# Optimization experiments

Hardware: AMD Instinct MI355X
Metric: run time of the kernel (lower is better)

Reference implementation:

```python
import jax, jax.numpy as jnp
import numpy as np

CURVS = (-1.0, 0.0, 1.0, -0.5)
N, E, B = 50000, 800000, 128
IN, HID, OUT, GHID = 128, 128, 128, 32
K = len(CURVS)
TAU_MIN, TAU_MAX = 0.05, 10.0
EPS = 1e-15


def _vnorm(x):
    return jnp.maximum(jnp.linalg.norm(x, axis=-1, keepdims=True), EPS)


def tan_k(x, k):
    if k > 0:
        sk = np.sqrt(k)
        return jnp.tan(x * sk) / sk
    if k < 0:
        sk = np.sqrt(-k)
        return jnp.tanh(x * sk) / sk
    return x


def artan_k(x, k):
    if k > 0:
        sk = np.sqrt(k)
        return jnp.arctan(x * sk) / sk
    if k < 0:
        sk = np.sqrt(-k)
        return jnp.arctanh(jnp.clip(x * sk, -1.0 + 1e-7, 1.0 - 1e-7)) / sk
    return x


def project(x, k):
    # clip inside Poincare ball for k<0; identity otherwise (geoopt Stereographic.projx)
    if k < 0:
        maxn = (1.0 - 1e-5) / np.sqrt(-k)
        n = _vnorm(x)
        return jnp.where(n > maxn, x * (maxn / n), x)
    return x


def expmap0(u, k):
    n = _vnorm(u)
    return project(tan_k(n, k) * u / n, k)


def logmap0(y, k):
    n = _vnorm(y)
    return artan_k(n, k) * y / n


def mobius_add(x, y, k):
    x2 = jnp.sum(x * x, -1, keepdims=True)
    y2 = jnp.sum(y * y, -1, keepdims=True)
    xy = jnp.sum(x * y, -1, keepdims=True)
    num = (1.0 - 2.0 * k * xy - k * y2) * x + (1.0 + k * x2) * y
    den = jnp.maximum(1.0 - 2.0 * k * xy + k * k * x2 * y2, 1e-15)
    return project(num / den, k)


def mobius_matvec(W, x, k):
    mx = x @ W.T
    if k == 0:
        return mx
    xn = _vnorm(x)
    mxn = _vnorm(mx)
    res = tan_k(mxn / xn * artan_k(xn, k), k) * mx / mxn
    res = jnp.where(jnp.sum(jnp.abs(mx), -1, keepdims=True) == 0.0, 0.0, res)
    return project(res, k)


def dist(x, y, k):
    return 2.0 * artan_k(_vnorm(mobius_add(-x, y, k)), k)[..., 0]


def setup_inputs():
    key = jax.random.key(0)
    ks = jax.random.split(key, 12)
    x = jax.random.normal(ks[0], (N, IN), jnp.float32)
    edge_index = jax.random.randint(ks[1], (2, E), 0, N)
    batch = jnp.sort(jax.random.randint(ks[2], (N,), 0, B))
    s1 = float(np.sqrt(2.0 / (IN + HID)))
    s2 = float(np.sqrt(2.0 / (HID + OUT)))
    sg1 = float(np.sqrt(2.0 / (IN + GHID)))
    sg2 = float(np.sqrt(2.0 / (GHID + OUT)))
    raw0 = float(np.log(np.expm1(1.0 - TAU_MIN)))
    return {
        "x": x,
        "edge_index": edge_index,
        "batch": batch,
        "expert_w1": jax.random.normal(ks[3], (K, HID, IN), jnp.float32) * s1,
        "expert_b1": jnp.zeros((K, HID), jnp.float32),
        "expert_w2": jax.random.normal(ks[4], (K, OUT, HID), jnp.float32) * s2,
        "expert_b2": jnp.zeros((K, OUT), jnp.float32),
        "gate_w1": jax.random.normal(ks[5], (GHID, IN), jnp.float32) * sg1,
        "gate_b1": jnp.zeros((GHID,), jnp.float32),
        "gate_w2": jax.random.normal(ks[6], (OUT, GHID), jnp.float32) * sg2,
        "gate_b2": jnp.zeros((OUT,), jnp.float32),
        "gate_u": jax.random.normal(ks[7], (K, OUT), jnp.float32) * 0.02,
        "tau_raw": jnp.full((K,), raw0, jnp.float32),
    }


def _graph_norm(edge_index):
    loops = jnp.arange(N)
    row = jnp.concatenate([edge_index[0], loops])
    col = jnp.concatenate([edge_index[1], loops])
    deg = jax.ops.segment_sum(jnp.ones(E + N, jnp.float32), col, num_segments=N)
    dinv = deg ** -0.5  # deg >= 1 due to self loops
    return row, col, dinv[row] * dinv[col]


def _kappa_conv(xm, W, b, row, col, enorm, k):
    h = mobius_matvec(W, xm, k)
    bias_pt = expmap0(b[None, :], k)  # proju at origin is identity
    h = mobius_add(h, bias_pt, k)
    t = logmap0(h, k)  # [N, out]
    agg = jax.ops.segment_sum(enorm[:, None] * t[row], col, num_segments=N)
    return expmap0(agg, k)


def reference(x, edge_index, batch, expert_w1, expert_b1, expert_w2, expert_b2,
              gate_w1, gate_b1, gate_w2, gate_b2, gate_u, tau_raw):
    x = x.astype(jnp.float32)
    row, col, enorm = _graph_norm(edge_index)
    counts = jnp.maximum(
        jax.ops.segment_sum(jnp.ones(N, jnp.float32), batch, num_segments=B), 1.0)[:, None]

    # --- Riemannian experts ---
    embs = []
    for i, kv in enumerate(CURVS):
        xm = expmap0(x, kv)  # manifold init (proju at origin = identity)
        xm = _kappa_conv(xm, expert_w1[i], expert_b1[i], row, col, enorm, kv)
        xm = _kappa_conv(xm, expert_w2[i], expert_b2[i], row, col, enorm, kv)
        z = logmap0(xm, kv)
        embs.append(jax.ops.segment_sum(z, batch, num_segments=B) / counts)
    features = jnp.concatenate(embs, axis=-1)  # [B, K*OUT]

    # --- Euclidean gating encoder (GCN) ---
    def gcn(h, W, b):
        m = (h @ W.T)
        out = jax.ops.segment_sum(enorm[:, None] * m[row], col, num_segments=N) + b
        return jax.nn.relu(out)

    g = gcn(x, gate_w1, gate_b1)
    g = gcn(g, gate_w2, gate_b2)
    hgate = jax.ops.segment_sum(g, batch, num_segments=B) / counts  # [B, OUT]

    # --- Geometric distance gate ---
    tau = jnp.clip(jax.nn.softplus(tau_raw) + TAU_MIN, TAU_MIN, TAU_MAX)
    dists = []
    for i, kv in enumerate(CURVS):
        zk = expmap0(hgate, kv)
        yk = expmap0(gate_u[i][None, :], kv)
        dists.append(dist(zk, yk, kv))
    dists = jnp.stack(dists, axis=-1)  # [B, K]
    weights = jax.nn.softmax(-dists / tau[None, :], axis=-1)

    scaled = features * jnp.repeat(weights, OUT, axis=1)
    return scaled, weights, dists, tau
```

## Files before the change

kernel.cpp:

```cpp
#include <hip/hip_runtime.h>
#include <math.h>

#define NN 50000
#define EE 800000
#define ETOT (EE + NN)
#define BB 128
#define DIM 128
#define GHID 32
#define CHUNK 128
#define NCHUNK ((ETOT + CHUNK - 1) / CHUNK)
#define SCB 196

typedef _Float16 f16;
typedef _Float16 f16x2 __attribute__((ext_vector_type(2)));
typedef _Float16 f16x8 __attribute__((ext_vector_type(8)));
typedef float f32x4 __attribute__((ext_vector_type(4)));

struct CurvPack {
  float k[4], sk[4], mx[4];
};

__device__ __forceinline__ float wsum64(float v) {
#pragma unroll
  for (int m = 32; m; m >>= 1) v += __shfl_xor(v, m, 64);
  return v;
}

__device__ __forceinline__ float tan_k_d(float x, float kv, float sk) {
  if (kv > 0.f) return tanf(x * sk) / sk;
  if (kv < 0.f) return tanhf(x * sk) / sk;
  return x;
}

__device__ __forceinline__ float artan_k_d(float x, float kv, float sk) {
  if (kv > 0.f) return atanf(x * sk) / sk;
  if (kv < 0.f) {
    float t = x * sk;
    t = fminf(fmaxf(t, -1.f + 1e-7f), 1.f - 1e-7f);
    return atanhf(t) / sk;
  }
  return x;
}
// ... 112 lines not shown
    int mid = (lo + hi) >> 1;
    if (bnode[mid] < v) lo = mid + 1; else hi = mid;
  }
  bslot[g] = lo;
}

__device__ __forceinline__ bool span_head(const int* bnode, const int* bslot, const int* off,
                                          int g, int& nd) {
  if (bslot[g] != g) return false;
  nd = bnode[g];
  int s = off[nd], e = off[nd + 1];
  return (s / CHUNK) != ((e - 1) / CHUNK);
}

__global__ void k_zeroc(const int* __restrict__ bnode, const int* __restrict__ bslot,
                        const int* __restrict__ off, float* __restrict__ aggc, int nchunk) {
  int g = blockIdx.x * 4 + (threadIdx.x >> 6);
  int lane = threadIdx.x & 63;
  if (g >= nchunk) return;
  int nd;
  if (!span_head(bnode, bslot, off, g, nd)) return;
  float2 z = make_float2(0.f, 0.f);
#pragma unroll
  for (int i = 0; i < 4; i++) ((float2*)aggc)[(size_t)g * 256 + i * 64 + lane] = z;
}

__global__ void k_place(const int* __restrict__ ei, const float* __restrict__ dinv,
                        int* __restrict__ cursor, int2* __restrict__ esw, int e, int n) {
  int i = blockIdx.x * 256 + threadIdx.x;
  int et = e + n;
  if (i >= et) return;
  int r_, c_;
  if (i < e) {
    r_ = ei[i];
    c_ = ei[e + i];
  } else {
    r_ = i - e;
    c_ = i - e;
  }
  int p = atomicAdd(&cursor[c_], 1);
  esw[p] = make_int2(r_, __float_as_int(dinv[r_] * dinv[c_]));
}

__global__ void k_nodeprep(const float* __restrict__ x, float* __restrict__ scl,
                           float* __restrict__ xnk, int n, CurvPack cp) {
  int wid = blockIdx.x * 4 + (threadIdx.x >> 6);
  int lane = threadIdx.x & 63;
  if (wid >= n) return;
  float2 v = ((const float2*)x)[(size_t)wid * 64 + lane];
  float n2 = wsum64(v.x * v.x + v.y * v.y);
  float nraw = sqrtf(n2);
  if (lane < 4) {
    float kv = cp.k[lane], sk = cp.sk[lane], maxn = cp.mx[lane];
    float nnv = fmaxf(nraw, 1e-15f);
    float tk = tan_k_d(nnv, kv, sk);
    float s = tk / nnv;
    float pn = fmaxf(fabsf(tk) * (nraw / nnv), 1e-15f);
    float ps = proj_scale_d(pn, kv, maxn);
    scl[(size_t)lane * n + wid] = s * ps;
    xnk[(size_t)lane * n + wid] = pn * ps;
  }
}

__global__ void k_biaspt_all(const float* __restrict__ eb1, const float* __restrict__ eb2,
                             float* __restrict__ biasb, CurvPack cp) {
  __shared__ float l2[2];
  int blk = blockIdx.x;
  int ex = blk >> 1, layer = blk & 1;
  float kv = cp.k[ex], sk = cp.sk[ex], maxn = cp.mx[ex];
  const float* b = (layer ? eb2 : eb1) + ex * 128;
  float* outb = biasb + blk * 132;
  int j = threadIdx.x;
  float v = b[j];
  float n2 = wsum64(v * v);
  if ((j & 63) == 0) l2[j >> 6] = n2;
  __syncthreads();
  n2 = l2[0] + l2[1];
  float nraw = sqrtf(n2);
  float nnv = fmaxf(nraw, 1e-15f);
  float tk = tan_k_d(nnv, kv, sk);
  float s = tk / nnv;
  float pn = fmaxf(fabsf(tk) * (nraw / nnv), 1e-15f);
  float ps = proj_scale_d(pn, kv, maxn);
  float bp = ps * s * v;
  outb[j] = bp;
  float y2v = wsum64(bp * bp);
  __syncthreads();
  if ((j & 63) == 0) l2[j >> 6] = y2v;
  __syncthreads();
  if (j == 0) outb[128] = l2[0] + l2[1];
}

__global__ void k_w2h(const float* __restrict__ ew1, const float* __restrict__ ew2,
                      f16* __restrict__ whi, f16* __restrict__ wlo) {
  int i = blockIdx.x * 256 + threadIdx.x;
  if (i >= 8 * 16384) return;
  int slot = i >> 14;
  int r = i & 16383;
  int ex = slot >> 1, layer = slot & 1;
  float w = (layer ? ew2 : ew1)[ex * 16384 + r];
  f16 h = (f16)w;
  whi[i] = h;
  wlo[i] = (f16)(w - (float)h);
}

__global__ __launch_bounds__(256) void k_matmfma(
    const float* __restrict__ A, int astr, int aoffPerEx, const float* __restrict__ sclB,
    const float* __restrict__ xnkB, const f16* __restrict__ whiB,
    const f16* __restrict__ wloB, const float* __restrict__ biasB, int layer,
    f16* __restrict__ tout, int n, CurvPack cp) {
  __shared__ float red[3][16][4];
  __shared__ float redT[16][4];
  __shared__ float nAs[16], nCs[16], nL[16];
  int ex = blockIdx.y;
  float kv = cp.k[ex], sk = cp.sk[ex], maxn = cp.mx[ex];
  const f16* whi = whiB + (size_t)(ex * 2 + layer) * 16384;
  const f16* wlo = wloB + (size_t)(ex * 2 + layer) * 16384;
  const float* biasb = biasB + (ex * 2 + layer) * 132;
  const float* scale = sclB + (size_t)ex * n;
  const float* xnorm = xnkB + (size_t)ex * n;

  int tid = threadIdx.x;
  int w = tid >> 6;
  int lane = tid & 63;
  int col = lane & 15;
  int quad = lane >> 4;
  int n0w = blockIdx.x * 16;
  if (n0w >= n) return;

  int anodec = min(n0w + col, n - 1);
  const float* arow = A + (size_t)anodec * astr + ex * aoffPerEx;
  int jt0 = w * 2;

  f32x4 acc[2];
  acc[0] = (f32x4){0.f, 0.f, 0.f, 0.f};
  acc[1] = (f32x4){0.f, 0.f, 0.f, 0.f};

#pragma unroll
  for (int kc = 0; kc < 4; kc++) {
    int kb = kc * 32 + quad * 8;
    float4 a0 = *(const float4*)(arow + kb);
    float4 a1 = *(const float4*)(arow + kb + 4);
    float av[8] = {a0.x, a0.y, a0.z, a0.w, a1.x, a1.y, a1.z, a1.w};
    f16x8 Ah, Al;
#pragma unroll
    for (int i = 0; i < 8; i++) {
      f16 h = (f16)av[i];
      Ah[i] = h;
      Al[i] = (f16)(av[i] - (float)h);
    }
#pragma unroll
    for (int j2 = 0; j2 < 2; j2++) {
      const f16* bh = whi + (size_t)((jt0 + j2) * 16 + col) * 128 + kb;
      const f16* bl = wlo + (size_t)((jt0 + j2) * 16 + col) * 128 + kb;
      f16x8 Bh = *(const f16x8*)bh;
      f16x8 Bl = *(const f16x8*)bl;
      acc[j2] = __builtin_amdgcn_mfma_f32_16x16x32_f16(Ah, Bh, acc[j2], 0, 0, 0);
      acc[j2] = __builtin_amdgcn_mfma_f32_16x16x32_f16(Ah, Bl, acc[j2], 0, 0, 0);
      acc[j2] = __builtin_amdgcn_mfma_f32_16x16x32_f16(Al, Bh, acc[j2], 0, 0, 0);
    }
  }

  float bpj[2];
  bpj[0] = biasb[jt0 * 16 + col];
  bpj[1] = biasb[(jt0 + 1) * 16 + col];
  float y2 = biasb[128];

#pragma unroll
  for (int r = 0; r < 4; r++) {
    float s0 = 0.f, s1 = 0.f, s2 = 0.f;
#pragma unroll
    for (int j2 = 0; j2 < 2; j2++) {
      float v = acc[j2][r];
      s0 = fmaf(v, v, s0);
      s1 += fabsf(v);
      s2 = fmaf(v, bpj[j2], s2);
    }
#pragma unroll
    for (int m = 1; m < 16; m <<= 1) {
      s0 += __shfl_xor(s0, m, 64);
      s1 += __shfl_xor(s1, m, 64);
      s2 += __shfl_xor(s2, m, 64);
    }
    if (col == 0) {
      red[0][quad * 4 + r][w] = s0;
      red[1][quad * 4 + r][w] = s1;
      red[2][quad * 4 + r][w] = s2;
    }
  }
  __syncthreads();

  if (tid < 16) {
    int gnode = min(n0w + tid, n - 1);
    float sc = scale[gnode];
    float s0f = (red[0][tid][0] + red[0][tid][1] + red[0][tid][2] + red[0][tid][3]) * sc * sc;
    float s1f = (red[1][tid][0] + red[1][tid][1] + red[1][tid][2] + red[1][tid][3]) * fabsf(sc);
    float s2f = (red[2][tid][0] + red[2][tid][1] + red[2][tid][2] + red[2][tid][3]) * sc;
    float xnr = xnorm[gnode];
    float xn = fmaxf(xnr, 1e-15f);
    float mxraw = sqrtf(s0f);
    float mxv = fmaxf(mxraw, 1e-15f);
    float ar = artan_k_d(xn, kv, sk);
    float c1 = tan_k_d(mxv / xn * ar, kv, sk);
    float s = (s1f == 0.f) ? 0.f : c1 / mxv;
    float pn = fmaxf(fabsf(c1) * (mxraw / mxv), 1e-15f);
    float ps = (s1f == 0.f) ? 1.f : proj_scale_d(pn, kv, maxn);
    s *= ps;
    float x2 = (s * s) * s0f;
    float xy = s * s2f;
    float Aa = 1.f - 2.f * kv * xy - kv * y2;
    float Cc = 1.f + kv * x2;
    float den = fmaxf(1.f - 2.f * kv * xy + (kv * kv) * x2 * y2, 1e-15f);
    nAs[tid] = Aa * s / den * sc;
    nCs[tid] = Cc / den;
  }
  __syncthreads();

#pragma unroll
  for (int r = 0; r < 4; r++) {
    int idx = quad * 4 + r;
    float Asc = nAs[idx], Cs = nCs[idx];
// ... 4 lines not shown
      t0 = fmaf(v, v, t0);
    }
#pragma unroll
    for (int m = 1; m < 16; m <<= 1) t0 += __shfl_xor(t0, m, 64);
    if (col == 0) redT[idx][w] = t0;
  }
  __syncthreads();

  if (tid < 16) {
    float t0f = redT[tid][0] + redT[tid][1] + redT[tid][2] + redT[tid][3];
    float nraw = sqrtf(t0f);
    float ps2 = proj_scale_d(fmaxf(nraw, 1e-15f), kv, maxn);
    float nh = fmaxf(ps2 * nraw, 1e-15f);
    nL[tid] = artan_k_d(nh, kv, sk) / nh * ps2;
  }
  __syncthreads();

#pragma unroll
  for (int r = 0; r < 4; r++) {
    int idx = quad * 4 + r;
    int gnode = n0w + idx;
    if (gnode >= n) continue;
    float Asc = nAs[idx], Cs = nCs[idx], L = nL[idx];
    f16* trow = tout + (size_t)gnode * 512 + ex * 128;
#pragma unroll
    for (int j2 = 0; j2 < 2; j2++) {
      float v = fmaf(Asc, acc[j2][r], Cs * bpj[j2]);
      trow[(jt0 + j2) * 16 + col] = (f16)(L * v);
    }
  }
}

template <int MODE, int NE>
__global__ __launch_bounds__(256) void k_aggF(
    const int2* __restrict__ esw, const int* __restrict__ off,
    const int* __restrict__ bnode, const int* __restrict__ bslot,
    const int* __restrict__ batch, const f16x2* __restrict__ t, float* __restrict__ agg1,
    float* __restrict__ aggc, float* __restrict__ scl2, float* __restrict__ xnk2,
    float* __restrict__ feats, const float* __restrict__ bias, float* __restrict__ hgate,
    int etot, int n, CurvPack cp) {
  int gw = blockIdx.x * 4 + (threadIdx.x >> 6);
  int lane = threadIdx.x & 63;
  int e0 = gw * CHUNK;
  if (e0 >= etot) return;
  int e1 = min(e0 + CHUNK, etot);
  int bnHead = bnode[gw];
  int slotA = bslot[gw];
  int slotB = ((gw + 1) * CHUNK < etot) ? bslot[gw + 1] : slotA;
  int cur = bnHead;
  int runStart = off[cur];
  int eend = off[cur + 1];
  float ax[NE], ay[NE], pax[NE], pay[NE];
#pragma unroll
  for (int e = 0; e < NE; e++) {
    ax[e] = ay[e] = pax[e] = pay[e] = 0.f;
  }
  int bcur = (MODE >= 1) ? batch[cur] : 0;
  float bbx = 0.f, bby = 0.f;
  if (MODE == 2) {
    float2 bb = ((const float2*)bias)[lane];
    bbx = bb.x;
    bby = bb.y;
  }

  auto flushInterior = [&]() {
#pragma unroll
    for (int e = 0; e < NE; e++) {
      if (MODE == 0) {
        ((float2*)agg1)[(size_t)cur * 256 + e * 64 + lane] = make_float2(ax[e], ay[e]);
        float n2 = wsum64(fmaf(ax[e], ax[e], ay[e] * ay[e]));
        float nraw = sqrtf(n2);
        float nnv = fmaxf(nraw, 1e-15f);
        float tk = tan_k_d(nnv, cp.k[e], cp.sk[e]);
        float s = tk / nnv;
        float pn = fmaxf(fabsf(tk) * (nraw / nnv), 1e-15f);
        float ps = proj_scale_d(pn, cp.k[e], cp.mx[e]);
        if (lane == 0) {
          scl2[(size_t)e * n + cur] = s * ps;
          xnk2[(size_t)e * n + cur] = pn * ps;
        }
      } else if (MODE == 1) {
        float n2 = wsum64(fmaf(ax[e], ax[e], ay[e] * ay[e]));
        float nraw = sqrtf(n2);
        float nnv = fmaxf(nraw, 1e-15f);
        float tk = tan_k_d(nnv, cp.k[e], cp.sk[e]);
        float s = tk / nnv;
        float pn = fmaxf(fabsf(tk) * (nraw / nnv), 1e-15f);
        float ps = proj_scale_d(pn, cp.k[e], cp.mx[e]);
        s *= ps;
        float nh = fmaxf(pn * ps, 1e-15f);
        float sc = artan_k_d(nh, cp.k[e], cp.sk[e]) / nh * s;
        pax[e] = fmaf(sc, ax[e], pax[e]);
        pay[e] = fmaf(sc, ay[e], pay[e]);
      } else {
        pax[e] += fmaxf(ax[e] + bbx, 0.f);
        pay[e] += fmaxf(ay[e] + bby, 0.f);
      }
    }
  };
  auto flushBoundary = [&]() {
    int slot = (cur == bnHead) ? slotA : slotB;
#pragma unroll
    for (int e = 0; e < NE; e++) {
      float* dp = aggc + (size_t)slot * 512 + e * 128 + lane * 2;
      atomicAdd(dp, ax[e]);
      atomicAdd(dp + 1, ay[e]);
    }
  };
  auto flushPool = [&]() {
#pragma unroll
    for (int e = 0; e < NE; e++) {
      if (MODE == 1) {
        float* fp = &feats[(size_t)bcur * 512 + e * 128 + lane * 2];
        atomicAdd(fp, pax[e]);
        atomicAdd(fp + 1, pay[e]);
      } else if (MODE == 2) {
        float* hp = &hgate[(size_t)bcur * 128 + lane * 2];
        atomicAdd(hp, pax[e]);
        atomicAdd(hp + 1, pay[e]);
      }
    }
  };

  int j = e0;
  while (j < e1) {
    if (j + 8 <= e1 && eend >= j + 8) {
      int2 m[8];
#pragma unroll
      for (int q = 0; q < 8; q++) m[q] = esw[j + q];
      f16x2 r[8][NE];
#pragma unroll
      for (int q = 0; q < 8; q++) {
        int s = __builtin_amdgcn_readfirstlane(m[q].x);
        const f16x2* base = t + (size_t)s * 256;
#pragma unroll
        for (int e = 0; e < NE; e++) r[q][e] = base[e * 64 + lane];
      }
#pragma unroll
      for (int q = 0; q < 8; q++) {
        float w = __int_as_float(m[q].y);
#pragma unroll
        for (int e = 0; e < NE; e++) {
          ax[e] = fmaf(w, (float)r[q][e][0], ax[e]);
          ay[e] = fmaf(w, (float)r[q][e][1], ay[e]);
        }
      }
      j += 8;
    } else if (j + 4 <= e1 && eend >= j + 4) {
      int2 m[4];
#pragma unroll
      for (int q = 0; q < 4; q++) m[q] = esw[j + q];
      f16x2 r[4][NE];
#pragma unroll
      for (int q = 0; q < 4; q++) {
        int s = __builtin_amdgcn_readfirstlane(m[q].x);
        const f16x2* base = t + (size_t)s * 256;
#pragma unroll
        for (int e = 0; e < NE; e++) r[q][e] = base[e * 64 + lane];
      }
#pragma unroll
      for (int q = 0; q < 4; q++) {
        float w = __int_as_float(m[q].y);
#pragma unroll
        for (int e = 0; e < NE; e++) {
          ax[e] = fmaf(w, (float)r[q][e][0], ax[e]);
          ay[e] = fmaf(w, (float)r[q][e][1], ay[e]);
        }
      }
      j += 4;
    } else {
      if (j == eend) {
        if (runStart >= e0) flushInterior(); else flushBoundary();
#pragma unroll
        for (int e = 0; e < NE; e++) ax[e] = ay[e] = 0.f;
        runStart = j;
        cur++;
        eend = off[cur + 1];
        if (MODE >= 1) {
          int nb = batch[cur];
          if (nb != bcur) {
            flushPool();
#pragma unroll
            for (int e = 0; e < NE; e++) pax[e] = pay[e] = 0.f;
            bcur = nb;
          }
        }
      }
      int2 m = esw[j];
      int s = __builtin_amdgcn_readfirstlane(m.x);
      const f16x2* base = t + (size_t)s * 256;
      float w = __int_as_float(m.y);
#pragma unroll
      for (int e = 0; e < NE; e++) {
        f16x2 rv = base[e * 64 + lane];
        ax[e] = fmaf(w, (float)rv[0], ax[e]);
        ay[e] = fmaf(w, (float)rv[1], ay[e]);
      }
      j++;
    }
  }
  if (runStart >= e0 && eend <= e1) flushInterior(); else flushBoundary();
  if (MODE >= 1) flushPool();
}

__global__ void k_fix1(const int* __restrict__ bnode, const int* __restrict__ bslot,
                       const int* __restrict__ off, const float* __restrict__ aggc,
                       float* __restrict__ agg1, float* __restrict__ scl2,
                       float* __restrict__ xnk2, int nchunk, int n, CurvPack cp) {
  int g = blockIdx.x * 4 + (threadIdx.x >> 6);
  int lane = threadIdx.x & 63;
  if (g >= nchunk) return;
  int nd;
  if (!span_head(bnode, bslot, off, g, nd)) return;
#pragma unroll
  for (int e = 0; e < 4; e++) {
    float2 v = ((const float2*)aggc)[(size_t)g * 256 + e * 64 + lane];
    ((float2*)agg1)[(size_t)nd * 256 + e * 64 + lane] = v;
    float n2 = wsum64(fmaf(v.x, v.x, v.y * v.y));
    float nraw = sqrtf(n2);
    float nnv = fmaxf(nraw, 1e-15f);
    float tk = tan_k_d(nnv, cp.k[e], cp.sk[e]);
    float s = tk / nnv;
    float pn = fmaxf(fabsf(tk) * (nraw / nnv), 1e-15f);
    float ps = proj_scale_d(pn, cp.k[e], cp.mx[e]);
    if (lane == 0) {
      scl2[(size_t)e * n + nd] = s * ps;
      xnk2[(size_t)e * n + nd] = pn * ps;
    }
  }
}

__global__ void k_fix2(const int* __restrict__ bnode, const int* __restrict__ bslot,
                       const int* __restrict__ off, const float* __restrict__ aggc,
                       const int* __restrict__ batch, float* __restrict__ feats, int nchunk,
                       CurvPack cp) {
  int g = blockIdx.x * 4 + (threadIdx.x >> 6);
  int lane = threadIdx.x & 63;
  if (g >= nchunk) return;
  int nd;
  if (!span_head(bnode, bslot, off, g, nd)) return;
  int b = batch[nd];
#pragma unroll
  for (int e = 0; e < 4; e++) {
    float2 v = ((const float2*)aggc)[(size_t)g * 256 + e * 64 + lane];
    float n2 = wsum64(fmaf(v.x, v.x, v.y * v.y));
    float nraw = sqrtf(n2);
    float nnv = fmaxf(nraw, 1e-15f);
    float tk = tan_k_d(nnv, cp.k[e], cp.sk[e]);
    float s = tk / nnv;
    float pn = fmaxf(fabsf(tk) * (nraw / nnv), 1e-15f);
    float ps = proj_scale_d(pn, cp.k[e], cp.mx[e]);
    s *= ps;
    float nh = fmaxf(pn * ps, 1e-15f);
    float sc = artan_k_d(nh, cp.k[e], cp.sk[e]) / nh * s;
    float* fp = &feats[(size_t)b * 512 + e * 128 + lane * 2];
    atomicAdd(fp, sc * v.x);
    atomicAdd(fp + 1, sc * v.y);
  }
}

__global__ void k_fixG(const int* __restrict__ bnode, const int* __restrict__ bslot,
                       const int* __restrict__ off, const float* __restrict__ aggc,
                       const int* __restrict__ batch, const float* __restrict__ bias,
                       float* __restrict__ hgate, int nchunk) {
  int g = blockIdx.x * 4 + (threadIdx.x >> 6);
  int lane = threadIdx.x & 63;
  if (g >= nchunk) return;
  int nd;
  if (!span_head(bnode, bslot, off, g, nd)) return;
  float2 v = ((const float2*)aggc)[(size_t)g * 256 + lane];
  float2 bb = ((const float2*)bias)[lane];
  int b = batch[nd];
  float* hp = &hgate[(size_t)b * 128 + lane * 2];
  atomicAdd(hp, fmaxf(v.x + bb.x, 0.f));
  atomicAdd(hp + 1, fmaxf(v.y + bb.y, 0.f));
}

__global__ __launch_bounds__(256) void k_gate1(const float* __restrict__ x,
                                               const float* __restrict__ gw1,
                                               float* __restrict__ m1, int n) {
  __shared__ float xT[64][68];
  __shared__ float Wt[64][36];
  int tid = threadIdx.x;
  int n0 = blockIdx.x * 64;
  int c = tid & 7, r = tid >> 3;
  float acc[2][4];
#pragma unroll
  for (int i = 0; i < 2; i++)
#pragma unroll
    for (int jj = 0; jj < 4; jj++) acc[i][jj] = 0.f;

  for (int kc = 0; kc < 2; kc++) {
    if (kc) __syncthreads();
#pragma unroll
    for (int it = 0; it < 8; it++) {
      int u = tid + it * 256;
      int j = u >> 6, kd = u & 63;
      Wt[kd][j] = gw1[j * 128 + kc * 64 + kd];
// ... 61 lines not shown
    xT[4 * c4 + 2][node] = v.z;
    xT[4 * c4 + 3][node] = v.w;
  }
  __syncthreads();
#pragma unroll 8
  for (int kd = 0; kd < 32; kd++) {
    float4 av = *(const float4*)&xT[kd][r * 4];
    float4 b0 = *(const float4*)&Wt[kd][c * 8];
    float4 b1 = *(const float4*)&Wt[kd][c * 8 + 4];
    float a[4] = {av.x, av.y, av.z, av.w};
    float bbv[8] = {b0.x, b0.y, b0.z, b0.w, b1.x, b1.y, b1.z, b1.w};
#pragma unroll
    for (int i = 0; i < 4; i++)
#pragma unroll
      for (int jj = 0; jj < 8; jj++) acc[i][jj] = fmaf(a[i], bbv[jj], acc[i][jj]);
  }
#pragma unroll
  for (int i = 0; i < 4; i++) {
    int node = n0 + r * 4 + i;
    if (node >= n) continue;
    f16x8 hv;
#pragma unroll
    for (int jj = 0; jj < 8; jj++) hv[jj] = (f16)acc[i][jj];
    *((f16x8*)(m2 + (size_t)node * 512) + c) = hv;
  }
}

__global__ void k_agg_relu32(const float* __restrict__ m1, const int* __restrict__ off,
                             const int2* __restrict__ esw, const float* __restrict__ bias,
                             float* __restrict__ g1, int n) {
  int node = blockIdx.x * 4 + (threadIdx.x >> 6);
  int lane = threadIdx.x & 63;
  if (node >= n) return;
  int grp = lane >> 3, l8 = lane & 7;
  int e0 = off[node], e1 = off[node + 1];
  float4 acc = make_float4(0.f, 0.f, 0.f, 0.f);
  for (int base = e0 + grp; base < e1; base += 8) {
    int2 me = esw[base];
    int ss = me.x;
    float ww = __int_as_float(me.y);
    float4 tv = ((const float4*)m1)[(size_t)ss * 8 + l8];
    acc.x = fmaf(ww, tv.x, acc.x);
    acc.y = fmaf(ww, tv.y, acc.y);
    acc.z = fmaf(ww, tv.z, acc.z);
    acc.w = fmaf(ww, tv.w, acc.w);
  }
#pragma unroll
  for (int m = 8; m <= 32; m <<= 1) {
    acc.x += __shfl_xor(acc.x, m, 64);
    acc.y += __shfl_xor(acc.y, m, 64);
    acc.z += __shfl_xor(acc.z, m, 64);
    acc.w += __shfl_xor(acc.w, m, 64);
  }
  if (grp == 0) {
    float4 bb = ((const float4*)bias)[l8];
    float4 o = make_float4(fmaxf(acc.x + bb.x, 0.f), fmaxf(acc.y + bb.y, 0.f),
                           fmaxf(acc.z + bb.z, 0.f), fmaxf(acc.w + bb.w, 0.f));
    ((float4*)g1)[(size_t)node * 8 + l8] = o;
  }
}

__global__ __launch_bounds__(128) void k_final(const float* __restrict__ feats,
                                               const float* __restrict__ hgate,
                                               const float* __restrict__ counts,
                                               const float* __restrict__ gate_u,
                                               const float* __restrict__ tau_raw,
                                               float* __restrict__ out, CurvPack cp) {
  __shared__ float l2[2];
  int b = blockIdx.x;
  int j = threadIdx.x;
  float cnt = fmaxf(counts[b], 1.f);
  float hg = hgate[(size_t)b * 128 + j] / cnt;

  auto bsum = [&](float v) -> float {
    v = wsum64(v);
    __syncthreads();
    if ((j & 63) == 0) l2[j >> 6] = v;
    __syncthreads();
    return l2[0] + l2[1];
  };

// ... 71 lines not shown
                              void* d_out, int out_size, void* d_ws, size_t ws_size,
                              hipStream_t stream) {
  const float* x = (const float*)d_in[0];
  const int* ei = (const int*)d_in[1];
  const int* batch = (const int*)d_in[2];
  const float* ew1 = (const float*)d_in[3];
  const float* eb1 = (const float*)d_in[4];
  const float* ew2 = (const float*)d_in[5];
  const float* eb2 = (const float*)d_in[6];
  const float* gw1 = (const float*)d_in[7];
  const float* gb1 = (const float*)d_in[8];
  const float* gw2 = (const float*)d_in[9];
  const float* gb2 = (const float*)d_in[10];
  const float* gu = (const float*)d_in[11];
  const float* traw = (const float*)d_in[12];
  float* out = (float*)d_out;

  const int N = NN, E = EE, ET = ETOT, B = BB;

  float* ws = (float*)d_ws;
  size_t o = 0;
  f16* t4 = (f16*)ws;       o += (size_t)N * 256;
  float* agg1 = ws + o;     o += (size_t)N * 512;
  float* aggc = ws + o;     o += (size_t)NCHUNK * 512;
  float* deg = ws + o;      o += N;
  float* scl1 = ws + o;     o += (size_t)4 * N;
  float* xnk1 = ws + o;     o += (size_t)4 * N;
  float* scl2 = ws + o;     o += (size_t)4 * N;
  float* xnk2 = ws + o;     o += (size_t)4 * N;
  float* counts = ws + o;   o += 256;
  float* feats = ws + o;    o += (size_t)B * 512;
  float* hg = ws + o;       o += (size_t)B * 128;
  float* biasb = ws + o;    o += 8 * 132;
  f16* whi = (f16*)(ws + o);    o += 8 * 16384 / 2;
  f16* wlo = (f16*)(ws + o);    o += 8 * 16384 / 2;
  int* ideg = (int*)(ws + o);   o += N;
  int* csroff = (int*)(ws + o); o += N + 8;
  int* cursor = (int*)(ws + o); o += N;
  int* boff = (int*)(ws + o);   o += 136;
  int* bsum = (int*)(ws + o);   o += 256;
  int* bnode = (int*)(ws + o);  o += NCHUNK + 8;
  int* bslot = (int*)(ws + o);  o += NCHUNK + 8;
  int2* esw = (int2*)(ws + o);  o += (size_t)2 * ET;

  float* m1 = agg1;
  float* g1 = agg1 + (size_t)N * 32;

  hipMemsetAsync(counts, 0, (256 + (size_t)B * 512 + (size_t)B * 128) * sizeof(float), stream);

  const double curvs[4] = {-1.0, 0.0, 1.0, -0.5};
  CurvPack cp;
  for (int i = 0; i < 4; i++) {
    double kd = curvs[i];
    double skd = sqrt(fabs(kd));
    cp.k[i] = (float)kd;
    cp.sk[i] = (float)skd;
    cp.mx[i] = (kd < 0) ? (float)((1.0 - 1e-5) / skd) : 3.0e38f;
  }

  k_init<<<(N + 255) / 256, 256, 0, stream>>>(deg, N);
  k_counts<<<1, 256, 0, stream>>>(batch, boff, counts, N);
  k_deg<<<(E + 255) / 256, 256, 0, stream>>>(ei, deg, E);
  k_dinv<<<(N + 255) / 256, 256, 0, stream>>>(deg, ideg, N);
  k_scanA<<<SCB, 256, 0, stream>>>(ideg, bsum, N);
  k_scanB<<<1, 256, 0, stream>>>(bsum, SCB);
  k_scanC<<<SCB, 256, 0, stream>>>(ideg, bsum, csroff, cursor, N);
  k_bnodes<<<(NCHUNK + 255) / 256, 256, 0, stream>>>(csroff, bnode, NCHUNK, N);
  k_bslot<<<(NCHUNK + 255) / 256, 256, 0, stream>>>(bnode, bslot, NCHUNK);
  k_place<<<(ET + 255) / 256, 256, 0, stream>>>(ei, deg, cursor, esw, E, N);
  k_nodeprep<<<(N + 3) / 4, 256, 0, stream>>>(x, scl1, xnk1, N, cp);
  k_biaspt_all<<<8, 128, 0, stream>>>(eb1, eb2, biasb, cp);
  k_w2h<<<512, 256, 0, stream>>>(ew1, ew2, whi, wlo);

  const int aggBlocks = (NCHUNK + 3) / 4;
  dim3 mfmaGrid((N + 15) / 16, 4);

  k_matmfma<<<mfmaGrid, 256, 0, stream>>>(x, 128, 0, scl1, xnk1, whi, wlo, biasb, 0, t4, N, cp);
  k_zeroc<<<aggBlocks, 256, 0, stream>>>(bnode, bslot, csroff, aggc, NCHUNK);
  k_aggF<0, 4><<<aggBlocks, 256, 0, stream>>>(esw, csroff, bnode, bslot, batch,
                                              (const f16x2*)t4, agg1, aggc, scl2, xnk2, nullptr,
                                              nullptr, nullptr, ET, N, cp);
  k_fix1<<<aggBlocks, 256, 0, stream>>>(bnode, bslot, csroff, aggc, agg1, scl2, xnk2, NCHUNK, N,
                                        cp);
  k_matmfma<<<mfmaGrid, 256, 0, stream>>>(agg1, 512, 128, scl2, xnk2, whi, wlo, biasb, 1, t4, N,
                                          cp);
  k_zeroc<<<aggBlocks, 256, 0, stream>>>(bnode, bslot, csroff, aggc, NCHUNK);
  k_aggF<1, 4><<<aggBlocks, 256, 0, stream>>>(esw, csroff, bnode, bslot, batch,
                                              (const f16x2*)t4, nullptr, aggc, nullptr, nullptr,
                                              feats, nullptr, nullptr, ET, N, cp);
  k_fix2<<<aggBlocks, 256, 0, stream>>>(bnode, bslot, csroff, aggc, batch, feats, NCHUNK, cp);

  k_gate1<<<(N + 63) / 64, 256, 0, stream>>>(x, gw1, m1, N);
  k_agg_relu32<<<(N + 3) / 4, 256, 0, stream>>>(m1, csroff, esw, gb1, g1, N);
  k_gate2<<<(N + 63) / 64, 256, 0, stream>>>(g1, gw2, t4, N);
  k_zeroc<<<aggBlocks, 256, 0, stream>>>(bnode, bslot, csroff, aggc, NCHUNK);
  k_aggF<2, 1><<<aggBlocks, 256, 0, stream>>>(esw, csroff, bnode, bslot, batch,
                                              (const f16x2*)t4, nullptr, aggc, nullptr, nullptr,
                                              nullptr, gb2, hg, ET, N, cp);
  k_fixG<<<aggBlocks, 256, 0, stream>>>(bnode, bslot, csroff, aggc, batch, gb2, hg, NCHUNK);

  k_final<<<B, 128, 0, stream>>>(feats, hg, counts, gu, traw, out, cp);

  (void)in_sizes; (void)n_in; (void)out_size; (void)ws_size;
}
```

Before: 1.016 ms.

## Fuse gate GCN aggregation into expert aggregation passes with interleaved feature layout

The Euclidean gate GCN's neighbour aggregations now run inside the two expert aggregation kernels, sharing the same edge walk. This removes the separate k_agg_relu32, gate-mode k_aggF and k_fixG launches and one full pass over the edge list. Per-node norms for the expmap scale are now computed inside the MFMA matmul instead of a separate prep kernel, which drops the scl/xnk buffers. The t4 output is interleaved so each lane fetches one 16-byte vector holding all four experts per neighbour. Edge metadata is loaded once per 8 edges and broadcast with readlane. When a node's norm is below a threshold where logmap(expmap(v)) is the identity, the transcendental round trip is skipped. This adds register pressure and more atomics in the boundary path.

```diff
diff --git a/kernel.cpp b/kernel.cpp
--- a/kernel.cpp
+++ b/kernel.cpp
@@ -17,7 +17,7 @@
 typedef float f32x4 __attribute__((ext_vector_type(4)));
 
 struct CurvPack {
-  float k[4], sk[4], mx[4];
+  float k[4], sk[4], mx[4], thr2[4];
 };
 
 __device__ __forceinline__ float wsum64(float v) {
@@ -176,7 +176,7 @@
   if (!span_head(bnode, bslot, off, g, nd)) return;
   float2 z = make_float2(0.f, 0.f);
 #pragma unroll
-  for (int i = 0; i < 4; i++) ((float2*)aggc)[(size_t)g * 256 + i * 64 + lane] = z;
+  for (int i = 0; i < 5; i++) ((float2*)aggc)[(size_t)g * 320 + i * 64 + lane] = z;
 }
 
 __global__ void k_place(const int* __restrict__ ei, const float* __restrict__ dinv,
@@ -196,26 +196,6 @@
   esw[p] = make_int2(r_, __float_as_int(dinv[r_] * dinv[c_]));
 }
 
-__global__ void k_nodeprep(const float* __restrict__ x, float* __restrict__ scl,
-                           float* __restrict__ xnk, int n, CurvPack cp) {
-  int wid = blockIdx.x * 4 + (threadIdx.x >> 6);
-  int lane = threadIdx.x & 63;
-  if (wid >= n) return;
-  float2 v = ((const float2*)x)[(size_t)wid * 64 + lane];
-  float n2 = wsum64(v.x * v.x + v.y * v.y);
-  float nraw = sqrtf(n2);
-  if (lane < 4) {
-    float kv = cp.k[lane], sk = cp.sk[lane], maxn = cp.mx[lane];
-    float nnv = fmaxf(nraw, 1e-15f);
-    float tk = tan_k_d(nnv, kv, sk);
-    float s = tk / nnv;
-    float pn = fmaxf(fabsf(tk) * (nraw / nnv), 1e-15f);
-    float ps = proj_scale_d(pn, kv, maxn);
-    scl[(size_t)lane * n + wid] = s * ps;
-    xnk[(size_t)lane * n + wid] = pn * ps;
-  }
-}
-
 __global__ void k_biaspt_all(const float* __restrict__ eb1, const float* __restrict__ eb2,
                              float* __restrict__ biasb, CurvPack cp) {
   __shared__ float l2[2];
@@ -259,10 +239,10 @@
 }
 
 __global__ __launch_bounds__(256) void k_matmfma(
-    const float* __restrict__ A, int astr, int aoffPerEx, const float* __restrict__ sclB,
-    const float* __restrict__ xnkB, const f16* __restrict__ whiB,
-    const f16* __restrict__ wloB, const float* __restrict__ biasB, int layer,
-    f16* __restrict__ tout, int n, CurvPack cp) {
+    const float* __restrict__ A, int astr, int aoffPerEx,
+    const f16* __restrict__ whiB, const f16* __restrict__ wloB,
+    const float* __restrict__ biasB, int layer, f16* __restrict__ tout, int n,
+    CurvPack cp) {
   __shared__ float red[3][16][4];
   __shared__ float redT[16][4];
   __shared__ float nAs[16], nCs[16], nL[16];
@@ -271,8 +251,6 @@
   const f16* whi = whiB + (size_t)(ex * 2 + layer) * 16384;
   const f16* wlo = wloB + (size_t)(ex * 2 + layer) * 16384;
   const float* biasb = biasB + (ex * 2 + layer) * 132;
-  const float* scale = sclB + (size_t)ex * n;
-  const float* xnorm = xnkB + (size_t)ex * n;
 
   int tid = threadIdx.x;
   int w = tid >> 6;
@@ -289,6 +267,7 @@
   f32x4 acc[2];
   acc[0] = (f32x4){0.f, 0.f, 0.f, 0.f};
   acc[1] = (f32x4){0.f, 0.f, 0.f, 0.f};
+  float a_n2 = 0.f;
 
 #pragma unroll
   for (int kc = 0; kc < 4; kc++) {
@@ -299,6 +278,7 @@
     f16x8 Ah, Al;
 #pragma unroll
     for (int i = 0; i < 8; i++) {
+      a_n2 = fmaf(av[i], av[i], a_n2);
       f16 h = (f16)av[i];
       Ah[i] = h;
       Al[i] = (f16)(av[i] - (float)h);
@@ -314,6 +294,8 @@
       acc[j2] = __builtin_amdgcn_mfma_f32_16x16x32_f16(Al, Bh, acc[j2], 0, 0, 0);
     }
   }
+  a_n2 += __shfl_xor(a_n2, 16, 64);
+  a_n2 += __shfl_xor(a_n2, 32, 64);
 
   float bpj[2];
   bpj[0] = biasb[jt0 * 16 + col];
@@ -345,12 +327,17 @@
   __syncthreads();
 
   if (tid < 16) {
-    int gnode = min(n0w + tid, n - 1);
-    float sc = scale[gnode];
+    float nraw0 = sqrtf(a_n2);
+    float nnv0 = fmaxf(nraw0, 1e-15f);
+    float tk0 = tan_k_d(nnv0, kv, sk);
+    float pn0 = fmaxf(fabsf(tk0) * (nraw0 / nnv0), 1e-15f);
+    float ps0 = proj_scale_d(pn0, kv, maxn);
+    float sc = (tk0 / nnv0) * ps0;
+    float xnr = pn0 * ps0;
+
     float s0f = (red[0][tid][0] + red[0][tid][1] + red[0][tid][2] + red[0][tid][3]) * sc * sc;
     float s1f = (red[1][tid][0] + red[1][tid][1] + red[1][tid][2] + red[1][tid][3]) * fabsf(sc);
     float s2f = (red[2][tid][0] + red[2][tid][1] + red[2][tid][2] + red[2][tid][3]) * sc;
-    float xnr = xnorm[gnode];
     float xn = fmaxf(xnr, 1e-15f);
     float mxraw = sqrtf(s0f);
     float mxv = fmaxf(mxraw, 1e-15f);
@@ -401,23 +388,26 @@
     int gnode = n0w + idx;
     if (gnode >= n) continue;
     float Asc = nAs[idx], Cs = nCs[idx], L = nL[idx];
-    f16* trow = tout + (size_t)gnode * 512 + ex * 128;
+    f16* trow = tout + (size_t)gnode * 512;
 #pragma unroll
     for (int j2 = 0; j2 < 2; j2++) {
       float v = fmaf(Asc, acc[j2][r], Cs * bpj[j2]);
-      trow[(jt0 + j2) * 16 + col] = (f16)(L * v);
-    }
-  }
-}
-
-template <int MODE, int NE>
+      int d = (jt0 + j2) * 16 + col;
+      trow[(d >> 1) * 8 + ex * 2 + (d & 1)] = (f16)(L * v);
+    }
+  }
+}
+
+template <int MODE>
 __global__ __launch_bounds__(256) void k_aggF(
     const int2* __restrict__ esw, const int* __restrict__ off,
     const int* __restrict__ bnode, const int* __restrict__ bslot,
-    const int* __restrict__ batch, const f16x2* __restrict__ t, float* __restrict__ agg1,
-    float* __restrict__ aggc, float* __restrict__ scl2, float* __restrict__ xnk2,
-    float* __restrict__ feats, const float* __restrict__ bias, float* __restrict__ hgate,
-    int etot, int n, CurvPack cp) {
+    const int* __restrict__ batch, const f16x8* __restrict__ t,
+    const float* __restrict__ gm1, const f16x2* __restrict__ tg,
+    float* __restrict__ agg1, float* __restrict__ aggc,
+    float* __restrict__ g1, float* __restrict__ feats,
+    const float* __restrict__ gbias, float* __restrict__ hgate,
+    int etot, CurvPack cp) {
   int gw = blockIdx.x * 4 + (threadIdx.x >> 6);
   int lane = threadIdx.x & 63;
   int e0 = gw * CHUNK;
@@ -429,199 +419,163 @@
   int cur = bnHead;
   int runStart = off[cur];
   int eend = off[cur + 1];
-  float ax[NE], ay[NE], pax[NE], pay[NE];
-#pragma unroll
-  for (int e = 0; e < NE; e++) {
-    ax[e] = ay[e] = pax[e] = pay[e] = 0.f;
-  }
-  int bcur = (MODE >= 1) ? batch[cur] : 0;
-  float bbx = 0.f, bby = 0.f;
-  if (MODE == 2) {
-    float2 bb = ((const float2*)bias)[lane];
+  float ax[4], ay[4], pax[4], pay[4];
+#pragma unroll
+  for (int e = 0; e < 4; e++) ax[e] = ay[e] = pax[e] = pay[e] = 0.f;
+  float gx = 0.f, gy = 0.f, pgx = 0.f, pgy = 0.f;
+  int bcur = (MODE == 1) ? batch[cur] : 0;
+  float bbx, bby = 0.f;
+  if (MODE == 0) {
+    bbx = gbias[lane & 31];
+  } else {
+    float2 bb = ((const float2*)gbias)[lane];
     bbx = bb.x;
     bby = bb.y;
   }
 
   auto flushInterior = [&]() {
 #pragma unroll
-    for (int e = 0; e < NE; e++) {
+    for (int e = 0; e < 4; e++) {
       if (MODE == 0) {
         ((float2*)agg1)[(size_t)cur * 256 + e * 64 + lane] = make_float2(ax[e], ay[e]);
+      } else {
         float n2 = wsum64(fmaf(ax[e], ax[e], ay[e] * ay[e]));
-        float nraw = sqrtf(n2);
-        float nnv = fmaxf(nraw, 1e-15f);
-        float tk = tan_k_d(nnv, cp.k[e], cp.sk[e]);
-        float s = tk / nnv;
-        float pn = fmaxf(fabsf(tk) * (nraw / nnv), 1e-15f);
-        float ps = proj_scale_d(pn, cp.k[e], cp.mx[e]);
-        if (lane == 0) {
-          scl2[(size_t)e * n + cur] = s * ps;
-          xnk2[(size_t)e * n + cur] = pn * ps;
+        if (n2 <= cp.thr2[e]) {
+          pax[e] += ax[e];
+          pay[e] += ay[e];
+        } else {
+          float nraw = sqrtf(n2);
+          float nnv = fmaxf(nraw, 1e-15f);
+          float tk = tan_k_d(nnv, cp.k[e], cp.sk[e]);
+          float s = tk / nnv;
+          float pn = fmaxf(fabsf(tk) * (nraw / nnv), 1e-15f);
+          float ps = proj_scale_d(pn, cp.k[e], cp.mx[e]);
+          s *= ps;
+          float nh = fmaxf(pn * ps, 1e-15f);
+          float sc = artan_k_d(nh, cp.k[e], cp.sk[e]) / nh * s;
+          pax[e] = fmaf(sc, ax[e], pax[e]);
+          pay[e] = fmaf(sc, ay[e], pay[e]);
         }
-      } else if (MODE == 1) {
-        float n2 = wsum64(fmaf(ax[e], ax[e], ay[e] * ay[e]));
-        float nraw = sqrtf(n2);
-        float nnv = fmaxf(nraw, 1e-15f);
-        float tk = tan_k_d(nnv, cp.k[e], cp.sk[e]);
-        float s = tk / nnv;
-        float pn = fmaxf(fabsf(tk) * (nraw / nnv), 1e-15f);
-        float ps = proj_scale_d(pn, cp.k[e], cp.mx[e]);
-        s *= ps;
-        float nh = fmaxf(pn * ps, 1e-15f);
-        float sc = artan_k_d(nh, cp.k[e], cp.sk[e]) / nh * s;
-        pax[e] = fmaf(sc, ax[e], pax[e]);
-        pay[e] = fmaf(sc, ay[e], pay[e]);
-      } else {
-        pax[e] += fmaxf(ax[e] + bbx, 0.f);
-        pay[e] += fmaxf(ay[e] + bby, 0.f);
       }
+    }
+    if (MODE == 0) {
+      if (lane < 32) g1[(size_t)cur * 32 + lane] = fmaxf(gx + bbx, 0.f);
+    } else {
+      pgx += fmaxf(gx + bbx, 0.f);
+      pgy += fmaxf(gy + bby, 0.f);
     }
   };
   auto flushBoundary = [&]() {
     int slot = (cur == bnHead) ? slotA : slotB;
-#pragma unroll
-    for (int e = 0; e < NE; e++) {
-      float* dp = aggc + (size_t)slot * 512 + e * 128 + lane * 2;
-      atomicAdd(dp, ax[e]);
-      atomicAdd(dp + 1, ay[e]);
+    float* dp = aggc + (size_t)slot * 640;
+#pragma unroll
+    for (int e = 0; e < 4; e++) {
+      atomicAdd(dp + e * 128 + lane * 2, ax[e]);
+      atomicAdd(dp + e * 128 + lane * 2 + 1, ay[e]);
+    }
+    if (MODE == 0) {
+      if (lane < 32) atomicAdd(dp + 512 + lane, gx);
+    } else {
+      atomicAdd(dp + 512 + lane * 2, gx);
+      atomicAdd(dp + 512 + lane * 2 + 1, gy);
     }
   };
   auto flushPool = [&]() {
 #pragma unroll
-    for (int e = 0; e < NE; e++) {
-      if (MODE == 1) {
-        float* fp = &feats[(size_t)bcur * 512 + e * 128 + lane * 2];
-        atomicAdd(fp, pax[e]);
-        atomicAdd(fp + 1, pay[e]);
-      } else if (MODE == 2) {
-        float* hp = &hgate[(size_t)bcur * 128 + lane * 2];
-        atomicAdd(hp, pax[e]);
-        atomicAdd(hp + 1, pay[e]);
-      }
-    }
+    for (int e = 0; e < 4; e++) {
+      float* fp = &feats[(size_t)bcur * 512 + e * 128 + lane * 2];
+      atomicAdd(fp, pax[e]);
+      atomicAdd(fp + 1, pay[e]);
+    }
+    float* hp = &hgate[(size_t)bcur * 128 + lane * 2];
+    atomicAdd(hp, pgx);
+    atomicAdd(hp + 1, pgy);
   };
 
-  int j = e0;
-  while (j < e1) {
-    if (j + 8 <= e1 && eend >= j + 8) {
-      int2 m[8];
-#pragma unroll
-      for (int q = 0; q < 8; q++) m[q] = esw[j + q];
-      f16x2 r[8][NE];
-#pragma unroll
-      for (int q = 0; q < 8; q++) {
-        int s = __builtin_amdgcn_readfirstlane(m[q].x);
-        const f16x2* base = t + (size_t)s * 256;
-#pragma unroll
-        for (int e = 0; e < NE; e++) r[q][e] = base[e * 64 + lane];
-      }
-#pragma unroll
-      for (int q = 0; q < 8; q++) {
-        float w = __int_as_float(m[q].y);
-#pragma unroll
-        for (int e = 0; e < NE; e++) {
-          ax[e] = fmaf(w, (float)r[q][e][0], ax[e]);
-          ay[e] = fmaf(w, (float)r[q][e][1], ay[e]);
-        }
-      }
-      j += 8;
-    } else if (j + 4 <= e1 && eend >= j + 4) {
-      int2 m[4];
-#pragma unroll
-      for (int q = 0; q < 4; q++) m[q] = esw[j + q];
-      f16x2 r[4][NE];
-#pragma unroll
-      for (int q = 0; q < 4; q++) {
-        int s = __builtin_amdgcn_readfirstlane(m[q].x);
-        const f16x2* base = t + (size_t)s * 256;
-#pragma unroll
-        for (int e = 0; e < NE; e++) r[q][e] = base[e * 64 + lane];
-      }
-#pragma unroll
-      for (int q = 0; q < 4; q++) {
-        float w = __int_as_float(m[q].y);
-#pragma unroll
-        for (int e = 0; e < NE; e++) {
-          ax[e] = fmaf(w, (float)r[q][e][0], ax[e]);
-          ay[e] = fmaf(w, (float)r[q][e][1], ay[e]);
-        }
-      }
-      j += 4;
-    } else {
-      if (j == eend) {
+  for (int j = e0; j < e1; j += 8) {
+    int2 mv = esw[j + (lane & 7)];
+    f16x8 rv[8];
+    float gvf[8];
+    f16x2 gvh[8];
+#pragma unroll
+    for (int q = 0; q < 8; q++) {
+      int s = __builtin_amdgcn_readlane(mv.x, q);
+      rv[q] = t[(size_t)s * 64 + lane];
+      if (MODE == 0) gvf[q] = gm1[(size_t)s * 32 + (lane & 31)];
+      else gvh[q] = tg[(size_t)s * 64 + lane];
+    }
+#pragma unroll
+    for (int q = 0; q < 8; q++) {
+      if (j + q == eend) {
         if (runStart >= e0) flushInterior(); else flushBoundary();
 #pragma unroll
-        for (int e = 0; e < NE; e++) ax[e] = ay[e] = 0.f;
-        runStart = j;
+        for (int e = 0; e < 4; e++) ax[e] = ay[e] = 0.f;
+        gx = gy = 0.f;
+        runStart = j + q;
         cur++;
         eend = off[cur + 1];
-        if (MODE >= 1) {
-          int nb = batch[cur];
-          if (nb != bcur) {
+        if (MODE == 1) {
+          int nbt = batch[cur];
+          if (nbt != bcur) {
             flushPool();
 #pragma unroll
-            for (int e = 0; e < NE; e++) pax[e] = pay[e] = 0.f;
-            bcur = nb;
+            for (int e = 0; e < 4; e++) pax[e] = pay[e] = 0.f;
+            pgx = pgy = 0.f;
+            bcur = nbt;
           }
         }
       }
-      int2 m = esw[j];
-      int s = __builtin_amdgcn_readfirstlane(m.x);
-      const f16x2* base = t + (size_t)s * 256;
-      float w = __int_as_float(m.y);
-#pragma unroll
-      for (int e = 0; e < NE; e++) {
-        f16x2 rv = base[e * 64 + lane];
-        ax[e] = fmaf(w, (float)rv[0], ax[e]);
-        ay[e] = fmaf(w, (float)rv[1], ay[e]);
+      float w = __int_as_float(__builtin_amdgcn_readlane(mv.y, q));
+#pragma unroll
+      for (int e = 0; e < 4; e++) {
+        ax[e] = fmaf(w, (float)rv[q][2 * e], ax[e]);
+        ay[e] = fmaf(w, (float)rv[q][2 * e + 1], ay[e]);
       }
-      j++;
+      if (MODE == 0) {
+        gx = fmaf(w, gvf[q], gx);
+      } else {
+        gx = fmaf(w, (float)gvh[q][0], gx);
+        gy = fmaf(w, (float)gvh[q][1], gy);
+      }
     }
   }
   if (runStart >= e0 && eend <= e1) flushInterior(); else flushBoundary();
-  if (MODE >= 1) flushPool();
+  if (MODE == 1) flushPool();
 }
 
 __global__ void k_fix1(const int* __restrict__ bnode, const int* __restrict__ bslot,
                        const int* __restrict__ off, const float* __restrict__ aggc,
-                       float* __restrict__ agg1, float* __restrict__ scl2,
-                       float* __restrict__ xnk2, int nchunk, int n, CurvPack cp) {
+                       float* __restrict__ agg1, float* __restrict__ g1,
+                       const float* __restrict__ gb1, int nchunk) {
   int g = blockIdx.x * 4 + (threadIdx.x >> 6);
   int lane = threadIdx.x & 63;
   if (g >= nchunk) return;
   int nd;
   if (!span_head(bnode, bslot, off, g, nd)) return;
+  const float* sp = aggc + (size_t)g * 640;
 #pragma unroll
   for (int e = 0; e < 4; e++) {
-    float2 v = ((const float2*)aggc)[(size_t)g * 256 + e * 64 + lane];
+    float2 v = ((const float2*)sp)[e * 64 + lane];
     ((float2*)agg1)[(size_t)nd * 256 + e * 64 + lane] = v;
-    float n2 = wsum64(fmaf(v.x, v.x, v.y * v.y));
-    float nraw = sqrtf(n2);
-    float nnv = fmaxf(nraw, 1e-15f);
-    float tk = tan_k_d(nnv, cp.k[e], cp.sk[e]);
-    float s = tk / nnv;
-    float pn = fmaxf(fabsf(tk) * (nraw / nnv), 1e-15f);
-    float ps = proj_scale_d(pn, cp.k[e], cp.mx[e]);
-    if (lane == 0) {
-      scl2[(size_t)e * n + nd] = s * ps;
-      xnk2[(size_t)e * n + nd] = pn * ps;
-    }
-  }
+  }
+  if (lane < 32) g1[(size_t)nd * 32 + lane] = fmaxf(sp[512 + lane] + gb1[lane], 0.f);
 }
 
 __global__ void k_fix2(const int* __restrict__ bnode, const int* __restrict__ bslot,
                        const int* __restrict__ off, const float* __restrict__ aggc,
-                       const int* __restrict__ batch, float* __restrict__ feats, int nchunk,
-                       CurvPack cp) {
+                       const int* __restrict__ batch, float* __restrict__ feats,
+                       const float* __restrict__ gb2, float* __restrict__ hgate,
+                       int nchunk, CurvPack cp) {
   int g = blockIdx.x * 4 + (threadIdx.x >> 6);
   int lane = threadIdx.x & 63;
   if (g >= nchunk) return;
   int nd;
   if (!span_head(bnode, bslot, off, g, nd)) return;
   int b = batch[nd];
+  const float* sp = aggc + (size_t)g * 640;
 #pragma unroll
   for (int e = 0; e < 4; e++) {
-    float2 v = ((const float2*)aggc)[(size_t)g * 256 + e * 64 + lane];
+    float2 v = ((const float2*)sp)[e * 64 + lane];
     float n2 = wsum64(fmaf(v.x, v.x, v.y * v.y));
     float nraw = sqrtf(n2);
     float nnv = fmaxf(nraw, 1e-15f);
@@ -636,23 +590,11 @@
     atomicAdd(fp, sc * v.x);
     atomicAdd(fp + 1, sc * v.y);
   }
-}
-
-__global__ void k_fixG(const int* __restrict__ bnode, const int* __restrict__ bslot,
-                       const int* __restrict__ off, const float* __restrict__ aggc,
-                       const int* __restrict__ batch, const float* __restrict__ bias,
-                       float* __restrict__ hgate, int nchunk) {
-  int g = blockIdx.x * 4 + (threadIdx.x >> 6);
-  int lane = threadIdx.x & 63;
-  if (g >= nchunk) return;
-  int nd;
-  if (!span_head(bnode, bslot, off, g, nd)) return;
-  float2 v = ((const float2*)aggc)[(size_t)g * 256 + lane];
-  float2 bb = ((const float2*)bias)[lane];
-  int b = batch[nd];
+  float2 gv = ((const float2*)(sp + 512))[lane];
+  float2 bb = ((const float2*)gb2)[lane];
   float* hp = &hgate[(size_t)b * 128 + lane * 2];
-  atomicAdd(hp, fmaxf(v.x + bb.x, 0.f));
-  atomicAdd(hp + 1, fmaxf(v.y + bb.y, 0.f));
+  atomicAdd(hp, fmaxf(gv.x + bb.x, 0.f));
+  atomicAdd(hp + 1, fmaxf(gv.y + bb.y, 0.f));
 }
 
 __global__ __launch_bounds__(256) void k_gate1(const float* __restrict__ x,
@@ -760,41 +702,7 @@
     f16x8 hv;
 #pragma unroll
     for (int jj = 0; jj < 8; jj++) hv[jj] = (f16)acc[i][jj];
-    *((f16x8*)(m2 + (size_t)node * 512) + c) = hv;
-  }
-}
-
-__global__ void k_agg_relu32(const float* __restrict__ m1, const int* __restrict__ off,
-                             const int2* __restrict__ esw, const float* __restrict__ bias,
-                             float* __restrict__ g1, int n) {
-  int node = blockIdx.x * 4 + (threadIdx.x >> 6);
-  int lane = threadIdx.x & 63;
-  if (node >= n) return;
-  int grp = lane >> 3, l8 = lane & 7;
-  int e0 = off[node], e1 = off[node + 1];
-  float4 acc = make_float4(0.f, 0.f, 0.f, 0.f);
-  for (int base = e0 + grp; base < e1; base += 8) {
-    int2 me = esw[base];
-    int ss = me.x;
-    float ww = __int_as_float(me.y);
-    float4 tv = ((const float4*)m1)[(size_t)ss * 8 + l8];
-    acc.x = fmaf(ww, tv.x, acc.x);
-    acc.y = fmaf(ww, tv.y, acc.y);
-    acc.z = fmaf(ww, tv.z, acc.z);
-    acc.w = fmaf(ww, tv.w, acc.w);
-  }
-#pragma unroll
-  for (int m = 8; m <= 32; m <<= 1) {
-    acc.x += __shfl_xor(acc.x, m, 64);
-    acc.y += __shfl_xor(acc.y, m, 64);
-    acc.z += __shfl_xor(acc.z, m, 64);
-    acc.w += __shfl_xor(acc.w, m, 64);
-  }
-  if (grp == 0) {
-    float4 bb = ((const float4*)bias)[l8];
-    float4 o = make_float4(fmaxf(acc.x + bb.x, 0.f), fmaxf(acc.y + bb.y, 0.f),
-                           fmaxf(acc.z + bb.z, 0.f), fmaxf(acc.w + bb.w, 0.f));
-    ((float4*)g1)[(size_t)node * 8 + l8] = o;
+    *((f16x8*)(m2 + (size_t)node * 128) + c) = hv;
   }
 }
 
@@ -912,18 +820,17 @@
   size_t o = 0;
   f16* t4 = (f16*)ws;       o += (size_t)N * 256;
   float* agg1 = ws + o;     o += (size_t)N * 512;
-  float* aggc = ws + o;     o += (size_t)NCHUNK * 512;
+  float* aggc = ws + o;     o += (size_t)NCHUNK * 640;
   float* deg = ws + o;      o += N;
-  float* scl1 = ws + o;     o += (size_t)4 * N;
-  float* xnk1 = ws + o;     o += (size_t)4 * N;
-  float* scl2 = ws + o;     o += (size_t)4 * N;
-  float* xnk2 = ws + o;     o += (size_t)4 * N;
   float* counts = ws + o;   o += 256;
   float* feats = ws + o;    o += (size_t)B * 512;
   float* hg = ws + o;       o += (size_t)B * 128;
   float* biasb = ws + o;    o += 8 * 132;
   f16* whi = (f16*)(ws + o);    o += 8 * 16384 / 2;
   f16* wlo = (f16*)(ws + o);    o += 8 * 16384 / 2;
+  float* m1 = ws + o;       o += (size_t)N * 32;
+  float* g1 = ws + o;       o += (size_t)N * 32;
+  f16* tg = (f16*)(ws + o); o += (size_t)N * 64;
   int* ideg = (int*)(ws + o);   o += N;
   int* csroff = (int*)(ws + o); o += N + 8;
   int* cursor = (int*)(ws + o); o += N;
@@ -933,9 +840,6 @@
   int* bslot = (int*)(ws + o);  o += NCHUNK + 8;
   int2* esw = (int2*)(ws + o);  o += (size_t)2 * ET;
 
-  float* m1 = agg1;
-  float* g1 = agg1 + (size_t)N * 32;
-
   hipMemsetAsync(counts, 0, (256 + (size_t)B * 512 + (size_t)B * 128) * sizeof(float), stream);
 
   const double curvs[4] = {-1.0, 0.0, 1.0, -0.5};
@@ -946,6 +850,15 @@
     cp.k[i] = (float)kd;
     cp.sk[i] = (float)skd;
     cp.mx[i] = (kd < 0) ? (float)((1.0 - 1e-5) / skd) : 3.0e38f;
+    if (kd < 0) {
+      double thr = 6.0 / skd;
+      cp.thr2[i] = (float)(thr * thr);
+    } else if (kd > 0) {
+      double thr = 1.5 / skd;
+      cp.thr2[i] = (float)(thr * thr);
+    } else {
+      cp.thr2[i] = 3.0e38f;
+    }
   }
 
   k_init<<<(N + 255) / 256, 256, 0, stream>>>(deg, N);
@@ -958,36 +871,28 @@
   k_bnodes<<<(NCHUNK + 255) / 256, 256, 0, stream>>>(csroff, bnode, NCHUNK, N);
   k_bslot<<<(NCHUNK + 255) / 256, 256, 0, stream>>>(bnode, bslot, NCHUNK);
   k_place<<<(ET + 255) / 256, 256, 0, stream>>>(ei, deg, cursor, esw, E, N);
-  k_nodeprep<<<(N + 3) / 4, 256, 0, stream>>>(x, scl1, xnk1, N, cp);
   k_biaspt_all<<<8, 128, 0, stream>>>(eb1, eb2, biasb, cp);
   k_w2h<<<512, 256, 0, stream>>>(ew1, ew2, whi, wlo);
+  k_gate1<<<(N + 63) / 64, 256, 0, stream>>>(x, gw1, m1, N);
 
   const int aggBlocks = (NCHUNK + 3) / 4;
   dim3 mfmaGrid((N + 15) / 16, 4);
 
-  k_matmfma<<<mfmaGrid, 256, 0, stream>>>(x, 128, 0, scl1, xnk1, whi, wlo, biasb, 0, t4, N, cp);
+  k_matmfma<<<mfmaGrid, 256, 0, stream>>>(x, 128, 0, whi, wlo, biasb, 0, t4, N, cp);
   k_zeroc<<<aggBlocks, 256, 0, stream>>>(bnode, bslot, csroff, aggc, NCHUNK);
-  k_aggF<0, 4><<<aggBlocks, 256, 0, stream>>>(esw, csroff, bnode, bslot, batch,
-                                              (const f16x2*)t4, agg1, aggc, scl2, xnk2, nullptr,
-                                              nullptr, nullptr, ET, N, cp);
-  k_fix1<<<aggBlocks, 256, 0, stream>>>(bnode, bslot, csroff, aggc, agg1, scl2, xnk2, NCHUNK, N,
-                                        cp);
-  k_matmfma<<<mfmaGrid, 256, 0, stream>>>(agg1, 512, 128, scl2, xnk2, whi, wlo, biasb, 1, t4, N,
-                                          cp);
+  k_aggF<0><<<aggBlocks, 256, 0, stream>>>(esw, csroff, bnode, bslot, batch,
+                                           (const f16x8*)t4, m1, nullptr, agg1, aggc, g1,
+                                           nullptr, gb1, nullptr, ET, cp);
+  k_fix1<<<aggBlocks, 256, 0, stream>>>(bnode, bslot, csroff, aggc, agg1, g1, gb1, NCHUNK);
+  k_gate2<<<(N + 63) / 64, 256, 0, stream>>>(g1, gw2, tg, N);
+
+  k_matmfma<<<mfmaGrid, 256, 0, stream>>>(agg1, 512, 128, whi, wlo, biasb, 1, t4, N, cp);
   k_zeroc<<<aggBlocks, 256, 0, stream>>>(bnode, bslot, csroff, aggc, NCHUNK);
-  k_aggF<1, 4><<<aggBlocks, 256, 0, stream>>>(esw, csroff, bnode, bslot, batch,
-                                              (const f16x2*)t4, nullptr, aggc, nullptr, nullptr,
-                                              feats, nullptr, nullptr, ET, N, cp);
-  k_fix2<<<aggBlocks, 256, 0, stream>>>(bnode, bslot, csroff, aggc, batch, feats, NCHUNK, cp);
-
-  k_gate1<<<(N + 63) / 64, 256, 0, stream>>>(x, gw1, m1, N);
-  k_agg_relu32<<<(N + 3) / 4, 256, 0, stream>>>(m1, csroff, esw, gb1, g1, N);
-  k_gate2<<<(N + 63) / 64, 256, 0, stream>>>(g1, gw2, t4, N);
-  k_zeroc<<<aggBlocks, 256, 0, stream>>>(bnode, bslot, csroff, aggc, NCHUNK);
-  k_aggF<2, 1><<<aggBlocks, 256, 0, stream>>>(esw, csroff, bnode, bslot, batch,
-                                              (const f16x2*)t4, nullptr, aggc, nullptr, nullptr,
-                                              nullptr, gb2, hg, ET, N, cp);
-  k_fixG<<<aggBlocks, 256, 0, stream>>>(bnode, bslot, csroff, aggc, batch, gb2, hg, NCHUNK);
+  k_aggF<1><<<aggBlocks, 256, 0, stream>>>(esw, csroff, bnode, bslot, batch,
+                                           (const f16x8*)t4, nullptr, (const f16x2*)tg,
+                                           nullptr, aggc, nullptr, feats, gb2, hg, ET, cp);
+  k_fix2<<<aggBlocks, 256, 0, stream>>>(bnode, bslot, csroff, aggc, batch, feats, gb2, hg,
+                                        NCHUNK, cp);
 
   k_final<<<B, 128, 0, stream>>>(feats, hg, counts, gu, traw, out, cp);
 
```

After: 960.1 us. 1.06x faster.
